# Optimization experiments

Measured on AMD Instinct MI355X. Metric: run time of the kernel, lower is better.

The kernel has to match this reference:

```python
import jax, jax.numpy as jnp
import numpy as np

N_NODES = 200000
N_EDGES = 6400000
IN_CH, HID, OUT_CH = 14, 16, 2


def gcn_conv(x, W, b, src, dst, n_nodes):
    """GCNConv with self-loops and symmetric normalization (PyG defaults).

    out[i] = sum_{j->i} d[i]^-1/2 d[j]^-1/2 (xW)[j] + d[i]^-1 (xW)[i] + b,
    where d = degree(A + I) computed on the target index.
    """
    h = x @ W  # [N, F_out]
    ones = jnp.ones((src.shape[0],), dtype=x.dtype)
    deg = jax.ops.segment_sum(ones, dst, num_segments=n_nodes) + 1.0  # +1 self-loop
    dinv = jax.lax.rsqrt(deg)  # [N]
    norm = dinv[src] * dinv[dst]  # [E]
    msg = h[src] * norm[:, None]  # [E, F_out] -- dominant memory traffic
    agg = jax.ops.segment_sum(msg, dst, num_segments=n_nodes)
    self_loop = h * (dinv * dinv)[:, None]
    return agg + self_loop + b


def setup_inputs() -> dict:
    key = jax.random.key(0)
    k1, k2, k3, k4, k5 = jax.random.split(key, 5)
    x = jax.random.normal(k1, (N_NODES, IN_CH), dtype=jnp.float32)
    edge_index = jax.random.randint(k2, (2, N_EDGES), 0, N_NODES, dtype=jnp.int64)
    edge_attr = jax.random.normal(k3, (N_EDGES, 1), dtype=jnp.float32)  # unused by GCNConv
    s = 1.0 / np.sqrt(IN_CH)
    W1 = jax.random.uniform(k4, (IN_CH, HID), jnp.float32, -s, s)
    b1 = jnp.zeros((HID,), jnp.float32)
    s2 = 1.0 / np.sqrt(HID)
    W2 = jax.random.uniform(k5, (HID, OUT_CH), jnp.float32, -s2, s2)
    b2 = jnp.zeros((OUT_CH,), jnp.float32)
    return {"x": x, "edge_index": edge_index, "edge_attr": edge_attr,
            "W1": W1, "b1": b1, "W2": W2, "b2": b2}


def reference(x, edge_index, edge_attr, W1, b1, W2, b2):
    src, dst = edge_index[0], edge_index[1]
    n = x.shape[0]
    h = jax.nn.relu(gcn_conv(x, W1, b1, src, dst, n))
    # F.dropout(training=self.training) is identity in eval mode
    out = gcn_conv(h, W2, b2, src, dst, n)
    return out
```

## Files before the change

kernel.cpp:

```cpp
#include <hip/hip_runtime.h>
#include <hip/hip_fp16.h>


constexpr int NN = 200000;
constexpr int NE = 6400000;
constexpr int IC = 14;
constexpr int HC = 16;
constexpr int OC = 2;

constexpr int NBK = 392;
constexpr int NSUB = 8;
constexpr int SCAP = 2816;
constexpr int NSEG = NSUB * NBK;
constexpr int CCAP = NSUB * SCAP;
constexpr int SPT = (SCAP + 1023) / 1024;
constexpr int TILE = 5120;
constexpr int BTH = 512;
constexpr int IPT = TILE / BTH;
constexpr int IPT2 = IPT / 2;
constexpr int NTILE = NE / TILE;
constexpr int OVFCAP = 65536;
constexpr int NB = (NN + 255) / 256;
constexpr int NAGG = NN / 64;
constexpr int GSTR = 16;

typedef unsigned long long ull;
typedef float f4v __attribute__((ext_vector_type(4)));

__device__ __forceinline__ int phase_of(unsigned src) {
    return src >= 100000u ? (src >= 150000u ? 3 : 2) : (src >= 50000u ? 1 : 0);
}

__global__ void k_init(int* __restrict__ gcur, const void* __restrict__ ei,
                       int* __restrict__ flag) {
    int i = blockIdx.x * blockDim.x + threadIdx.x;
    if (i < NSEG) gcur[i * GSTR] = i * SCAP;
    else if (i == NSEG) gcur[i * GSTR] = 0;
    if (i == 500) {
        const ull* p = (const ull*)ei;
        ull acc = 0ULL;
        for (int k = 0; k < 64; ++k) acc |= (p[k] >> 32);
        *flag = (acc == 0ULL) ? 1 : 0;
    }
}

__global__ __launch_bounds__(BTH, 8) void k_binA(const void* __restrict__ ei,
                                                 const int* __restrict__ flag,
                                                 int* __restrict__ gcur,
                                                 unsigned* __restrict__ binned,
                                                 ull* __restrict__ ovf) {
    __shared__ int hist[NBK];
    __shared__ int lofs[NBK];
    __shared__ int gofs[NBK];
    __shared__ int wsum[BTH / 64];
    __shared__ unsigned stage[TILE];

    int t = threadIdx.x;
    int fl = *flag;
    int tile0 = blockIdx.x * TILE;
    int segbase = (blockIdx.x & (NSUB - 1)) * NBK;

    if (t < NBK) hist[t] = 0;
    __syncthreads();

    unsigned pk[IPT];
    unsigned ra[IPT];
#pragma unroll
    for (int k = 0; k < IPT2; ++k) {
        int e = tile0 + k * (2 * BTH) + 2 * t;
        int d0, d1, s0, s1;
        if (fl) {
            ulonglong2 dd = *(const ulonglong2*)((const long long*)ei + NE + e);
            ulonglong2 ss = *(const ulonglong2*)((const long long*)ei + e);
            d0 = (int)dd.x;
            d1 = (int)dd.y;
            s0 = (int)ss.x;
            s1 = (int)ss.y;
        } else {
            uint2 dd = *(const uint2*)((const int*)ei + NE + e);
            uint2 ss = *(const uint2*)((const int*)ei + e);
            d0 = (int)dd.x;
            d1 = (int)dd.y;
            s0 = (int)ss.x;
            s1 = (int)ss.y;
        }
        int b0 = d0 >> 9, b1 = d1 >> 9;
        int r0 = atomicAdd(&hist[b0], 1);
        int r1 = atomicAdd(&hist[b1], 1);
        pk[2 * k] = ((unsigned)(d0 & 511) << 18) | (unsigned)s0;
        pk[2 * k + 1] = ((unsigned)(d1 & 511) << 18) | (unsigned)s1;
        ra[2 * k] = ((unsigned)r0 << 9) | (unsigned)b0;
        ra[2 * k + 1] = ((unsigned)r1 << 9) | (unsigned)b1;
    }
    __syncthreads();

    int h0 = 0, h1 = 0, p = 0;
    if (t < NBK / 2) {
        h0 = hist[2 * t];
        h1 = hist[2 * t + 1];
        p = h0 + h1;
    }
    int lane = t & 63;
    int w = t >> 6;
    int incl = p;
#pragma unroll
    for (int off = 1; off < 64; off <<= 1) {
        int v = __shfl_up(incl, off, 64);
        if (lane >= off) incl += v;
    }
    if (lane == 63) wsum[w] = incl;
    __syncthreads();
    int wbase = 0;
#pragma unroll
    for (int ww = 0; ww < BTH / 64; ++ww) wbase += (ww < w) ? wsum[ww] : 0;
    int ex = wbase + incl - p;
    if (t < NBK / 2) {
        lofs[2 * t] = ex;
        lofs[2 * t + 1] = ex + h0;
    }
    if (t < NBK) gofs[t] = atomicAdd(&gcur[(segbase + t) * GSTR], hist[t]);
    __syncthreads();

#pragma unroll
    for (int k = 0; k < IPT; ++k) {
        int b = (int)(ra[k] & 511u);
        int r = (int)(ra[k] >> 9);
        stage[lofs[b] + r] = pk[k];
    }
    __syncthreads();

    for (int i = t; i < TILE; i += BTH) {
        int b = (i * 313) >> 12;
        if (b > NBK - 1) b = NBK - 1;
        while (b < NBK - 1 && lofs[b + 1] <= i) ++b;
        while (lofs[b] > i) --b;
        unsigned pack = stage[i];
        int seg = segbase + b;
        int dest = gofs[b] + (i - lofs[b]);
        if (dest < (seg + 1) * SCAP) {
            binned[dest] = pack;
        } else {
            int op = atomicAdd(&gcur[NSEG * GSTR], 1);
            if (op < OVFCAP) {
                int d = (b << 9) | (int)(pack >> 18);
                int s = (int)(pack & 0x3FFFF);
                ovf[op] = ((ull)d << 32) | (unsigned)s;
            }
        }
    }
}

__global__ __launch_bounds__(1024, 4) void k_sort(const int* __restrict__ gcur,
                                                  const unsigned* __restrict__ binned,
                                                  const ull* __restrict__ ovf,
                                                  unsigned* __restrict__ csr,
                                                  float* __restrict__ dinv,
                                                  int* __restrict__ rsg,
                                                  unsigned* __restrict__ spl) {
    __shared__ int cnt[2048];
    __shared__ int excl[2048];
    __shared__ int wsum[16];
    __shared__ int nseg[NSUB];
    __shared__ unsigned stage[CCAP];
    int b = blockIdx.x;
    int t = threadIdx.x;
    cnt[t] = 0;
    cnt[t + 1024] = 0;
    if (t < NSUB) {
        int seg = t * NBK + b;
        nseg[t] = min(gcur[seg * GSTR] - seg * SCAP, SCAP);
    }
    __syncthreads();
    int nov = min(gcur[NSEG * GSTR], OVFCAP);

    unsigned srcv[NSUB * SPT];
    unsigned rkv[NSUB * SPT];
#pragma unroll
    for (int s = 0; s < NSUB; ++s) {
        int n = nseg[s];
        int sb = (s * NBK + b) * SCAP;
#pragma unroll
        for (int k = 0; k < SPT; ++k) {
            int i = k * 1024 + t;
            rkv[s * SPT + k] = 0xFFFFFFFFu;
            if (i < n) {
                unsigned pack = binned[sb + i];
                unsigned src = pack & 0x3FFFFu;
                int key = ((int)(pack >> 18) << 2) | phase_of(src);
                int r = atomicAdd(&cnt[key], 1);
                srcv[s * SPT + k] = src;
                rkv[s * SPT + k] = ((unsigned)r << 11) | (unsigned)key;
            }
        }
    }
    __syncthreads();

    int h0 = cnt[2 * t];
    int h1 = cnt[2 * t + 1];
    int p = h0 + h1;
    int lane = t & 63;
    int w = t >> 6;
    int incl = p;
#pragma unroll
    for (int off = 1; off < 64; off <<= 1) {
        int v = __shfl_up(incl, off, 64);
        if (lane >= off) incl += v;
    }
    if (lane == 63) wsum[w] = incl;
    __syncthreads();
    int wbase = 0;
#pragma unroll
    for (int ww = 0; ww < 16; ++ww) wbase += (ww < w) ? wsum[ww] : 0;
    int ex = wbase + incl - p;
    excl[2 * t] = ex;
    excl[2 * t + 1] = ex + h0;
    __syncthreads();

#pragma unroll
    for (int c = 0; c < NSUB * SPT; ++c) {
        unsigned rk = rkv[c];
        if (rk != 0xFFFFFFFFu) {
            int key = (int)(rk & 0x7FFu);
            int r = (int)(rk >> 11);
            stage[excl[key] + r] = srcv[c];
        }
    }

    if (t < 512) {
        int g = (b << 9) + t;
        if (g < NN) {
            int c0 = cnt[4 * t];
            int c1 = cnt[4 * t + 1];
            int c2 = cnt[4 * t + 2];
            int c3 = cnt[4 * t + 3];
            int extra = 0;
            for (int k = 0; k < nov; ++k) extra += ((int)(ovf[k] >> 32) == g);
            dinv[g] = rsqrtf((float)(c0 + c1 + c2 + c3 + extra) + 1.0f);
            rsg[g] = b * CCAP + excl[4 * t];
            spl[g] = (unsigned)c0 | ((unsigned)c1 << 8) |
                     ((unsigned)c2 << 16) | ((unsigned)c3 << 24);
        }
    }
    __syncthreads();

    int total = excl[2047] + cnt[2047];
    int tot4 = (total + 3) >> 2;
    const uint4* st4 = (const uint4*)stage;
    uint4* csr4 = (uint4*)(csr + (size_t)b * CCAP);
#pragma unroll
    for (int k = 0; k < (CCAP / 4 + 1023) / 1024; ++k) {
        int i4 = k * 1024 + t;
        if (i4 < tot4) csr4[i4] = st4[i4];
    }
}

__global__ void k_prep(const float* __restrict__ x, const float* __restrict__ dinv,
                       __half* __restrict__ xph) {
    int i = blockIdx.x * blockDim.x + threadIdx.x;
    if (i >= NN * 16) return;
    int node = i >> 4;
    int c = i & 15;
    float v = (c < IC) ? dinv[node] * x[node * IC + c] : 0.0f;
    xph[i] = __float2half(v);
}

__global__ __launch_bounds__(256) void k_agg1(const int* __restrict__ rsg,
                                              const unsigned* __restrict__ spl,
                                              const unsigned* __restrict__ csr,
                                              const __half* __restrict__ xph,
                                              float* __restrict__ partial,
                                              int pbase, int acc) {
    int t = threadIdx.x;
    int q2 = blockIdx.x & 1;
    int ph = pbase + q2;
    int blk = blockIdx.x >> 1;
    int g = t >> 2;
    int qq = t & 3;
    int i = blk * 64 + g;
    unsigned sp = spl[i];
    int c0 = (int)(sp & 255u);
    int c1 = (int)((sp >> 8) & 255u);
    int c2 = (int)((sp >> 16) & 255u);
    int c3 = (int)(sp >> 24);
    int off = (ph > 0 ? c0 : 0) + (ph > 1 ? c1 : 0) + (ph > 2 ? c2 : 0);
    int len = ph == 0 ? c0 : ph == 1 ? c1 : ph == 2 ? c2 : c3;
    int beg = rsg[i] + off;
    int end = beg + len;

    float ax = 0.0f, ay = 0.0f, az = 0.0f, aw = 0.0f;
    int j = beg;
    for (; j + 1 < end; j += 2) {
        int s0 = csr[j];
        int s1 = csr[j + 1];
        uint2 u0 = *(const uint2*)(xph + (size_t)s0 * 16 + 4 * qq);
        uint2 u1 = *(const uint2*)(xph + (size_t)s1 * 16 + 4 * qq);
        float2 f0 = __half22float2(*(__half2*)&u0.x);
        float2 f1 = __half22float2(*(__half2*)&u0.y);
        float2 f2 = __half22float2(*(__half2*)&u1.x);
        float2 f3 = __half22float2(*(__half2*)&u1.y);
        ax += f0.x + f2.x;
        ay += f0.y + f2.y;
        az += f1.x + f3.x;
        aw += f1.y + f3.y;
    }
    if (j < end) {
        int s0 = csr[j];
        uint2 u0 = *(const uint2*)(xph + (size_t)s0 * 16 + 4 * qq);
        float2 f0 = __half22float2(*(__half2*)&u0.x);
        float2 f1 = __half22float2(*(__half2*)&u0.y);
        ax += f0.x;
        ay += f0.y;
        az += f1.x;
        aw += f1.y;
    }
    f4v r = {ax, ay, az, aw};
    float* dst = partial + ((size_t)q2 * NN + i) * 16 + 4 * qq;
    if (acc) {
        f4v o = __builtin_nontemporal_load((const f4v*)dst);
        r += o;
    }
    __builtin_nontemporal_store(r, (f4v*)dst);
}

__global__ __launch_bounds__(256) void k_mlp(const float* __restrict__ partial,
                                             const __half* __restrict__ xph,
                                             const int* __restrict__ gcur,
                                             const ull* __restrict__ ovf,
                                             const float* __restrict__ dinv,
                                             const float* __restrict__ W1,
                                             const float* __restrict__ b1,
                                             const float* __restrict__ W2,
                                             const float* __restrict__ b2,
                                             float2* __restrict__ h2bp,
                                             float2* __restrict__ selfout) {
    __shared__ float sW1[IC * HC];
    __shared__ float sb1[HC];
    __shared__ float sW2[HC * OC];
    __shared__ float sb2[OC];
    int t = threadIdx.x;
    if (t < IC * HC) sW1[t] = W1[t];
    if (t < HC) sb1[t] = b1[t];
    if (t < HC * OC) sW2[t] = W2[t];
    if (t < OC) sb2[t] = b2[t];
    __syncthreads();

    int i = blockIdx.x * 256 + t;
    if (i >= NN) return;

    float dv = dinv[i];
    const float4* p0 = (const float4*)(partial + (size_t)i * 16);
    const float4* p1 = (const float4*)(partial + ((size_t)NN + i) * 16);
    const uint2* sp = (const uint2*)(xph + (size_t)i * 16);

    float agg[16];
#pragma unroll
    for (int c4 = 0; c4 < 4; ++c4) {
        float4 a = p0[c4];
        float4 b = p1[c4];
        uint2 u = sp[c4];
        float2 s0 = __half22float2(*(__half2*)&u.x);
        float2 s1 = __half22float2(*(__half2*)&u.y);
        agg[4 * c4 + 0] = a.x + b.x + s0.x;
        agg[4 * c4 + 1] = a.y + b.y + s0.y;
        agg[4 * c4 + 2] = a.z + b.z + s1.x;
        agg[4 * c4 + 3] = a.w + b.w + s1.y;
    }

    int nov = min(gcur[NSEG * GSTR], OVFCAP);
    for (int k = 0; k < nov; ++k) {
        ull e = ovf[k];
        if ((int)(e >> 32) == i) {
            int s = (int)(e & 0xFFFFFFFFu);
            for (int c = 0; c < IC; ++c)
                agg[c] += __half2float(xph[(size_t)s * 16 + c]);
        }
    }

    float tt[IC];
#pragma unroll
    for (int c = 0; c < IC; ++c) tt[c] = dv * agg[c];

    float r[HC];
#pragma unroll
    for (int f = 0; f < HC; ++f) {
        float a = sb1[f];
#pragma unroll
        for (int c = 0; c < IC; ++c) a = fmaf(tt[c], sW1[c * HC + f], a);
        r[f] = fmaxf(a, 0.0f);
    }

    float o0 = 0.0f, o1 = 0.0f;
#pragma unroll
    for (int f = 0; f < HC; ++f) {
        o0 = fmaf(r[f], sW2[f * OC + 0], o0);
        o1 = fmaf(r[f], sW2[f * OC + 1], o1);
    }
    h2bp[i] = make_float2(o0 * dv, o1 * dv);
    selfout[i] = make_float2(o0 * dv * dv + sb2[0], o1 * dv * dv + sb2[1]);
}

__global__ __launch_bounds__(256) void k_agg2(const int* __restrict__ rsg,
                                              const unsigned* __restrict__ spl,
                                              const unsigned* __restrict__ csr,
                                              const int* __restrict__ gcur,
                                              const ull* __restrict__ ovf,
                                              const float* __restrict__ dinv,
                                              const float2* __restrict__ h2bp,
                                              const float2* __restrict__ selfout,
                                              float2* __restrict__ out) {
    int tt = blockIdx.x * 256 + threadIdx.x;
    int i = tt >> 2;
    int h = tt & 3;
    if (i >= NN) return;
    unsigned sp = spl[i];
    int tot = (int)(sp & 255u) + (int)((sp >> 8) & 255u) +
              (int)((sp >> 16) & 255u) + (int)(sp >> 24);
    int beg = rsg[i];
    int end = beg + tot;
    float ax = 0.0f, ay = 0.0f;
    int j = beg + h;
    for (; j + 4 < end; j += 8) {
        int s0 = csr[j];
        int s1 = csr[j + 4];
        float2 h0 = h2bp[s0];
        float2 h1 = h2bp[s1];
        ax += h0.x + h1.x;
        ay += h0.y + h1.y;
    }
    if (j < end) {
        float2 h0 = h2bp[csr[j]];
        ax += h0.x;
        ay += h0.y;
    }
    ax += __shfl_xor(ax, 1);
    ay += __shfl_xor(ay, 1);
    ax += __shfl_xor(ax, 2);
    ay += __shfl_xor(ay, 2);
    if (h == 0) {
        int nov = min(gcur[NSEG * GSTR], OVFCAP);
        for (int k = 0; k < nov; ++k) {
            ull e = ovf[k];
            if ((int)(e >> 32) == i) {
                float2 hh = h2bp[(int)(e & 0xFFFFFFFFu)];
                ax += hh.x;
                ay += hh.y;
            }
        }
        float dv = dinv[i];
        float2 so = selfout[i];
        out[i] = make_float2(so.x + dv * ax, so.y + dv * ay);
    }
}

extern "C" void kernel_launch(void* const* d_in, const int* in_sizes, int n_in,
                              void* d_out, int out_size, void* d_ws, size_t ws_size,
                              hipStream_t stream) {
    const float* x = (const float*)d_in[0];
    const void* ei = d_in[1];
    const float* W1 = (const float*)d_in[3];
    const float* b1 = (const float*)d_in[4];
    const float* W2 = (const float*)d_in[5];
    const float* b2 = (const float*)d_in[6];
    float* out = (float*)d_out;

    ull* ovf = (ull*)d_ws;
    int* gcur = (int*)(ovf + OVFCAP);
    int* flag = gcur + (NSEG + 1) * GSTR;
    int* rsg = flag + 4;
    unsigned* spl = (unsigned*)(rsg + NN);
    float* dinv = (float*)(spl + NN);
    __half* xph = (__half*)(dinv + NN);
    float2* h2bp = (float2*)(xph + (size_t)NN * 16);
    float2* selfout = h2bp + NN;
    unsigned* binned = (unsigned*)(selfout + NN);
    float* partial = (float*)binned;
    unsigned* csr = binned + (size_t)NSEG * SCAP;

    k_init<<<(NSEG + 1 + 255) / 256, 256, 0, stream>>>(gcur, ei, flag);
    k_binA<<<NTILE, BTH, 0, stream>>>(ei, flag, gcur, binned, ovf);
    k_sort<<<NBK, 1024, 0, stream>>>(gcur, binned, ovf, csr, dinv, rsg, spl);
    k_prep<<<(NN * 16 + 255) / 256, 256, 0, stream>>>(x, dinv, xph);
    k_agg1<<<2 * NAGG, 256, 0, stream>>>(rsg, spl, csr, xph, partial, 0, 0);
    k_agg1<<<2 * NAGG, 256, 0, stream>>>(rsg, spl, csr, xph, partial, 2, 1);
    k_mlp<<<NB, 256, 0, stream>>>(partial, xph, gcur, ovf, dinv, W1, b1, W2, b2,
                                  h2bp, selfout);
    k_agg2<<<(NN * 4 + 255) / 256, 256, 0, stream>>>(rsg, spl, csr, gcur, ovf, dinv,
                                                     h2bp, selfout, (float2*)out);
}
```

Before: 308.5 us.

## Make binning and aggregation XCC-aware via hardware XCC id and atomic work claiming

The binning kernel now picks its sub-segment from the hardware XCC id instead of the block index, so each chiplet writes into its own bin region. The aggregation kernel replaces static block-to-phase mapping with an atomic work counter: blocks on XCCs 0-3 prefer one source-range phase and XCCs 4-7 the other, falling back to the other counter when theirs is exhausted. The goal is to keep each half of the gathered feature table resident in the local L2/cache of the chiplets processing it. This adds per-block atomics and a block-wide sync, and the number of blocks per bin region now depends on how the hardware distributes work across XCCs, so a skewed distribution could overflow a region's fixed capacity.

```diff
diff --git a/kernel.cpp b/kernel.cpp
--- a/kernel.cpp
+++ b/kernel.cpp
@@ -31,11 +31,17 @@
     return src >= 100000u ? (src >= 150000u ? 3 : 2) : (src >= 50000u ? 1 : 0);
 }
 
+__device__ __forceinline__ int xcc_id() {
+    int x;
+    asm volatile("s_getreg_b32 %0, hwreg(HW_REG_XCC_ID)" : "=s"(x));
+    return x & 7;
+}
+
 __global__ void k_init(int* __restrict__ gcur, const void* __restrict__ ei,
                        int* __restrict__ flag) {
     int i = blockIdx.x * blockDim.x + threadIdx.x;
     if (i < NSEG) gcur[i * GSTR] = i * SCAP;
-    else if (i == NSEG) gcur[i * GSTR] = 0;
+    else if (i <= NSEG + 4) gcur[i * GSTR] = 0;
     if (i == 500) {
         const ull* p = (const ull*)ei;
         ull acc = 0ULL;
@@ -58,7 +64,7 @@
     int t = threadIdx.x;
     int fl = *flag;
     int tile0 = blockIdx.x * TILE;
-    int segbase = (blockIdx.x & (NSUB - 1)) * NBK;
+    int segbase = xcc_id() * NBK;
 
     if (t < NBK) hist[t] = 0;
     __syncthreads();
@@ -269,11 +275,28 @@
                                               const unsigned* __restrict__ csr,
                                               const __half* __restrict__ xph,
                                               float* __restrict__ partial,
-                                              int pbase, int acc) {
+                                              int* __restrict__ gcur,
+                                              int pbase, int cbase, int acc) {
+    __shared__ int sw[2];
     int t = threadIdx.x;
-    int q2 = blockIdx.x & 1;
+    if (t == 0) {
+        int* cur = gcur + (NSEG + 1 + cbase) * GSTR;
+        int pref = (xcc_id() >> 2) & 1;
+        int idx = atomicAdd(&cur[pref * GSTR], 1);
+        int p = pref;
+        if (idx >= NAGG) {
+            p = pref ^ 1;
+            idx = atomicAdd(&cur[p * GSTR], 1);
+        }
+        sw[0] = idx;
+        sw[1] = p;
+    }
+    __syncthreads();
+    int blk = sw[0];
+    if (blk >= NAGG) return;
+    int q2 = sw[1];
     int ph = pbase + q2;
-    int blk = blockIdx.x >> 1;
+
     int g = t >> 2;
     int qq = t & 3;
     int i = blk * 64 + g;
@@ -314,7 +337,7 @@
         aw += f1.y;
     }
     f4v r = {ax, ay, az, aw};
-    float* dst = partial + ((size_t)q2 * NN + i) * 16 + 4 * qq;
+    float* dst = partial + ((size_t)(ph & 1) * NN + i) * 16 + 4 * qq;
     if (acc) {
         f4v o = __builtin_nontemporal_load((const f4v*)dst);
         r += o;
@@ -465,7 +488,7 @@
 
     ull* ovf = (ull*)d_ws;
     int* gcur = (int*)(ovf + OVFCAP);
-    int* flag = gcur + (NSEG + 1) * GSTR;
+    int* flag = gcur + (NSEG + 5) * GSTR;
     int* rsg = flag + 4;
     unsigned* spl = (unsigned*)(rsg + NN);
     float* dinv = (float*)(spl + NN);
@@ -476,12 +499,12 @@
     float* partial = (float*)binned;
     unsigned* csr = binned + (size_t)NSEG * SCAP;
 
-    k_init<<<(NSEG + 1 + 255) / 256, 256, 0, stream>>>(gcur, ei, flag);
+    k_init<<<(NSEG + 5 + 255) / 256, 256, 0, stream>>>(gcur, ei, flag);
     k_binA<<<NTILE, BTH, 0, stream>>>(ei, flag, gcur, binned, ovf);
     k_sort<<<NBK, 1024, 0, stream>>>(gcur, binned, ovf, csr, dinv, rsg, spl);
     k_prep<<<(NN * 16 + 255) / 256, 256, 0, stream>>>(x, dinv, xph);
-    k_agg1<<<2 * NAGG, 256, 0, stream>>>(rsg, spl, csr, xph, partial, 0, 0);
-    k_agg1<<<2 * NAGG, 256, 0, stream>>>(rsg, spl, csr, xph, partial, 2, 1);
+    k_agg1<<<2 * NAGG, 256, 0, stream>>>(rsg, spl, csr, xph, partial, gcur, 0, 0, 0);
+    k_agg1<<<2 * NAGG, 256, 0, stream>>>(rsg, spl, csr, xph, partial, gcur, 2, 2, 1);
     k_mlp<<<NB, 256, 0, stream>>>(partial, xph, gcur, ovf, dinv, W1, b1, W2, b2,
                                   h2bp, selfout);
     k_agg2<<<(NN * 4 + 255) / 256, 256, 0, stream>>>(rsg, spl, csr, gcur, ovf, dinv,
```

New measurement: 354.2 us. 14.8% more time.

## Fuse second aggregation pass with MLP and bin edges by XCC id

Applied to the files above, without the earlier changes.

The second layer-1 aggregation launch (source-range phases 2 and 3) is merged with the per-node MLP kernel into one kernel. Four threads per node gather the remaining phases, add the two stored partials and the self term, and compute the 16-wide hidden layer and 2-wide output cooperatively via shared memory and lane shuffles. This drops one launch and the read-modify-write of the partial buffer. Separately, the binning kernel now picks its sub-segment from the hardware XCC id instead of the block index, meant to keep atomic cursor traffic local to one chiplet. In exchange, the phase 2 and 3 gather no longer splits into two blocks per node group, so that part of the work runs with less parallelism.

```diff
diff --git a/kernel.cpp b/kernel.cpp
--- a/kernel.cpp
+++ b/kernel.cpp
@@ -20,7 +20,6 @@
 constexpr int IPT2 = IPT / 2;
 constexpr int NTILE = NE / TILE;
 constexpr int OVFCAP = 65536;
-constexpr int NB = (NN + 255) / 256;
 constexpr int NAGG = NN / 64;
 constexpr int GSTR = 16;
 
@@ -29,13 +28,19 @@
 
 __device__ __forceinline__ int phase_of(unsigned src) {
     return src >= 100000u ? (src >= 150000u ? 3 : 2) : (src >= 50000u ? 1 : 0);
+}
+
+__device__ __forceinline__ int xcc_id() {
+    int x;
+    asm volatile("s_getreg_b32 %0, hwreg(HW_REG_XCC_ID)" : "=s"(x));
+    return x & 7;
 }
 
 __global__ void k_init(int* __restrict__ gcur, const void* __restrict__ ei,
                        int* __restrict__ flag) {
     int i = blockIdx.x * blockDim.x + threadIdx.x;
     if (i < NSEG) gcur[i * GSTR] = i * SCAP;
-    else if (i == NSEG) gcur[i * GSTR] = 0;
+    else if (i <= NSEG + 4) gcur[i * GSTR] = 0;
     if (i == 500) {
         const ull* p = (const ull*)ei;
         ull acc = 0ULL;
@@ -58,7 +63,7 @@
     int t = threadIdx.x;
     int fl = *flag;
     int tile0 = blockIdx.x * TILE;
-    int segbase = (blockIdx.x & (NSUB - 1)) * NBK;
+    int segbase = xcc_id() * NBK;
 
     if (t < NBK) hist[t] = 0;
     __syncthreads();
@@ -268,11 +273,9 @@
                                               const unsigned* __restrict__ spl,
                                               const unsigned* __restrict__ csr,
                                               const __half* __restrict__ xph,
-                                              float* __restrict__ partial,
-                                              int pbase, int acc) {
+                                              float* __restrict__ partial) {
     int t = threadIdx.x;
     int q2 = blockIdx.x & 1;
-    int ph = pbase + q2;
     int blk = blockIdx.x >> 1;
     int g = t >> 2;
     int qq = t & 3;
@@ -280,12 +283,8 @@
     unsigned sp = spl[i];
     int c0 = (int)(sp & 255u);
     int c1 = (int)((sp >> 8) & 255u);
-    int c2 = (int)((sp >> 16) & 255u);
-    int c3 = (int)(sp >> 24);
-    int off = (ph > 0 ? c0 : 0) + (ph > 1 ? c1 : 0) + (ph > 2 ? c2 : 0);
-    int len = ph == 0 ? c0 : ph == 1 ? c1 : ph == 2 ? c2 : c3;
-    int beg = rsg[i] + off;
-    int end = beg + len;
+    int beg = rsg[i] + (q2 ? c0 : 0);
+    int end = beg + (q2 ? c1 : c0);
 
     float ax = 0.0f, ay = 0.0f, az = 0.0f, aw = 0.0f;
     int j = beg;
@@ -314,89 +313,122 @@
         aw += f1.y;
     }
     f4v r = {ax, ay, az, aw};
-    float* dst = partial + ((size_t)q2 * NN + i) * 16 + 4 * qq;
-    if (acc) {
-        f4v o = __builtin_nontemporal_load((const f4v*)dst);
-        r += o;
-    }
-    __builtin_nontemporal_store(r, (f4v*)dst);
-}
-
-__global__ __launch_bounds__(256) void k_mlp(const float* __restrict__ partial,
-                                             const __half* __restrict__ xph,
-                                             const int* __restrict__ gcur,
-                                             const ull* __restrict__ ovf,
-                                             const float* __restrict__ dinv,
-                                             const float* __restrict__ W1,
-                                             const float* __restrict__ b1,
-                                             const float* __restrict__ W2,
-                                             const float* __restrict__ b2,
-                                             float2* __restrict__ h2bp,
-                                             float2* __restrict__ selfout) {
+    __builtin_nontemporal_store(r, (f4v*)(partial + ((size_t)q2 * NN + i) * 16 + 4 * qq));
+}
+
+__global__ __launch_bounds__(256) void k_agg1m(const int* __restrict__ rsg,
+                                               const unsigned* __restrict__ spl,
+                                               const unsigned* __restrict__ csr,
+                                               const __half* __restrict__ xph,
+                                               const float* __restrict__ partial,
+                                               const int* __restrict__ gcur,
+                                               const ull* __restrict__ ovf,
+                                               const float* __restrict__ dinv,
+                                               const float* __restrict__ W1,
+                                               const float* __restrict__ b1,
+                                               const float* __restrict__ W2,
+                                               const float* __restrict__ b2,
+                                               float2* __restrict__ h2bp,
+                                               float2* __restrict__ selfout) {
     __shared__ float sW1[IC * HC];
     __shared__ float sb1[HC];
     __shared__ float sW2[HC * OC];
     __shared__ float sb2[OC];
+    __shared__ float sAgg[64][17];
     int t = threadIdx.x;
     if (t < IC * HC) sW1[t] = W1[t];
     if (t < HC) sb1[t] = b1[t];
     if (t < HC * OC) sW2[t] = W2[t];
     if (t < OC) sb2[t] = b2[t];
-    __syncthreads();
-
-    int i = blockIdx.x * 256 + t;
-    if (i >= NN) return;
-
-    float dv = dinv[i];
-    const float4* p0 = (const float4*)(partial + (size_t)i * 16);
-    const float4* p1 = (const float4*)(partial + ((size_t)NN + i) * 16);
-    const uint2* sp = (const uint2*)(xph + (size_t)i * 16);
-
-    float agg[16];
-#pragma unroll
-    for (int c4 = 0; c4 < 4; ++c4) {
-        float4 a = p0[c4];
-        float4 b = p1[c4];
-        uint2 u = sp[c4];
-        float2 s0 = __half22float2(*(__half2*)&u.x);
-        float2 s1 = __half22float2(*(__half2*)&u.y);
-        agg[4 * c4 + 0] = a.x + b.x + s0.x;
-        agg[4 * c4 + 1] = a.y + b.y + s0.y;
-        agg[4 * c4 + 2] = a.z + b.z + s1.x;
-        agg[4 * c4 + 3] = a.w + b.w + s1.y;
-    }
+
+    int g = t >> 2;
+    int qq = t & 3;
+    int i = blockIdx.x * 64 + g;
+    unsigned sp = spl[i];
+    int c0 = (int)(sp & 255u);
+    int c1 = (int)((sp >> 8) & 255u);
+    int c2 = (int)((sp >> 16) & 255u);
+    int c3 = (int)(sp >> 24);
+    int beg = rsg[i] + c0 + c1;
+    int end = beg + c2 + c3;
+
+    float ax = 0.0f, ay = 0.0f, az = 0.0f, aw = 0.0f;
+    int j = beg;
+    for (; j + 1 < end; j += 2) {
+        int s0 = csr[j];
+        int s1 = csr[j + 1];
+        uint2 u0 = *(const uint2*)(xph + (size_t)s0 * 16 + 4 * qq);
+        uint2 u1 = *(const uint2*)(xph + (size_t)s1 * 16 + 4 * qq);
+        float2 f0 = __half22float2(*(__half2*)&u0.x);
+        float2 f1 = __half22float2(*(__half2*)&u0.y);
+        float2 f2 = __half22float2(*(__half2*)&u1.x);
+        float2 f3 = __half22float2(*(__half2*)&u1.y);
+        ax += f0.x + f2.x;
+        ay += f0.y + f2.y;
+        az += f1.x + f3.x;
+        aw += f1.y + f3.y;
+    }
+    if (j < end) {
+        int s0 = csr[j];
+        uint2 u0 = *(const uint2*)(xph + (size_t)s0 * 16 + 4 * qq);
+        float2 f0 = __half22float2(*(__half2*)&u0.x);
+        float2 f1 = __half22float2(*(__half2*)&u0.y);
+        ax += f0.x;
+        ay += f0.y;
+        az += f1.x;
+        aw += f1.y;
+    }
+
+    f4v a0 = __builtin_nontemporal_load((const f4v*)(partial + (size_t)i * 16 + 4 * qq));
+    f4v a1 = __builtin_nontemporal_load(
+        (const f4v*)(partial + ((size_t)NN + i) * 16 + 4 * qq));
+    uint2 us = *(const uint2*)(xph + (size_t)i * 16 + 4 * qq);
+    float2 sx = __half22float2(*(__half2*)&us.x);
+    float2 sy = __half22float2(*(__half2*)&us.y);
+    float v0 = ax + a0.x + a1.x + sx.x;
+    float v1 = ay + a0.y + a1.y + sx.y;
+    float v2 = az + a0.z + a1.z + sy.x;
+    float v3 = aw + a0.w + a1.w + sy.y;
 
     int nov = min(gcur[NSEG * GSTR], OVFCAP);
     for (int k = 0; k < nov; ++k) {
         ull e = ovf[k];
         if ((int)(e >> 32) == i) {
             int s = (int)(e & 0xFFFFFFFFu);
-            for (int c = 0; c < IC; ++c)
-                agg[c] += __half2float(xph[(size_t)s * 16 + c]);
-        }
-    }
-
-    float tt[IC];
-#pragma unroll
-    for (int c = 0; c < IC; ++c) tt[c] = dv * agg[c];
-
-    float r[HC];
-#pragma unroll
-    for (int f = 0; f < HC; ++f) {
+            int ch = 4 * qq;
+            v0 += __half2float(xph[(size_t)s * 16 + ch]);
+            v1 += __half2float(xph[(size_t)s * 16 + ch + 1]);
+            v2 += __half2float(xph[(size_t)s * 16 + ch + 2]);
+            v3 += __half2float(xph[(size_t)s * 16 + ch + 3]);
+        }
+    }
+
+    float dv = dinv[i];
+    sAgg[g][4 * qq + 0] = dv * v0;
+    sAgg[g][4 * qq + 1] = dv * v1;
+    sAgg[g][4 * qq + 2] = dv * v2;
+    sAgg[g][4 * qq + 3] = dv * v3;
+    __syncthreads();
+
+    float o0 = 0.0f, o1 = 0.0f;
+#pragma unroll
+    for (int f4 = 0; f4 < 4; ++f4) {
+        int f = 4 * qq + f4;
         float a = sb1[f];
 #pragma unroll
-        for (int c = 0; c < IC; ++c) a = fmaf(tt[c], sW1[c * HC + f], a);
-        r[f] = fmaxf(a, 0.0f);
-    }
-
-    float o0 = 0.0f, o1 = 0.0f;
-#pragma unroll
-    for (int f = 0; f < HC; ++f) {
-        o0 = fmaf(r[f], sW2[f * OC + 0], o0);
-        o1 = fmaf(r[f], sW2[f * OC + 1], o1);
-    }
-    h2bp[i] = make_float2(o0 * dv, o1 * dv);
-    selfout[i] = make_float2(o0 * dv * dv + sb2[0], o1 * dv * dv + sb2[1]);
+        for (int c = 0; c < IC; ++c) a = fmaf(sAgg[g][c], sW1[c * HC + f], a);
+        a = fmaxf(a, 0.0f);
+        o0 = fmaf(a, sW2[f * OC + 0], o0);
+        o1 = fmaf(a, sW2[f * OC + 1], o1);
+    }
+    o0 += __shfl_xor(o0, 1);
+    o1 += __shfl_xor(o1, 1);
+    o0 += __shfl_xor(o0, 2);
+    o1 += __shfl_xor(o1, 2);
+    if (qq == 0) {
+        h2bp[i] = make_float2(o0 * dv, o1 * dv);
+        selfout[i] = make_float2(o0 * dv * dv + sb2[0], o1 * dv * dv + sb2[1]);
+    }
 }
 
 __global__ __launch_bounds__(256) void k_agg2(const int* __restrict__ rsg,
@@ -465,7 +497,7 @@
 
     ull* ovf = (ull*)d_ws;
     int* gcur = (int*)(ovf + OVFCAP);
-    int* flag = gcur + (NSEG + 1) * GSTR;
+    int* flag = gcur + (NSEG + 5) * GSTR;
     int* rsg = flag + 4;
     unsigned* spl = (unsigned*)(rsg + NN);
     float* dinv = (float*)(spl + NN);
@@ -476,14 +508,13 @@
     float* partial = (float*)binned;
     unsigned* csr = binned + (size_t)NSEG * SCAP;
 
-    k_init<<<(NSEG + 1 + 255) / 256, 256, 0, stream>>>(gcur, ei, flag);
+    k_init<<<(NSEG + 5 + 255) / 256, 256, 0, stream>>>(gcur, ei, flag);
     k_binA<<<NTILE, BTH, 0, stream>>>(ei, flag, gcur, binned, ovf);
     k_sort<<<NBK, 1024, 0, stream>>>(gcur, binned, ovf, csr, dinv, rsg, spl);
     k_prep<<<(NN * 16 + 255) / 256, 256, 0, stream>>>(x, dinv, xph);
-    k_agg1<<<2 * NAGG, 256, 0, stream>>>(rsg, spl, csr, xph, partial, 0, 0);
-    k_agg1<<<2 * NAGG, 256, 0, stream>>>(rsg, spl, csr, xph, partial, 2, 1);
-    k_mlp<<<NB, 256, 0, stream>>>(partial, xph, gcur, ovf, dinv, W1, b1, W2, b2,
-                                  h2bp, selfout);
+    k_agg1<<<2 * NAGG, 256, 0, stream>>>(rsg, spl, csr, xph, partial);
+    k_agg1m<<<NAGG, 256, 0, stream>>>(rsg, spl, csr, xph, partial, gcur, ovf, dinv,
+                                      W1, b1, W2, b2, h2bp, selfout);
     k_agg2<<<(NN * 4 + 255) / 256, 256, 0, stream>>>(rsg, spl, csr, gcur, ovf, dinv,
                                                      h2bp, selfout, (float2*)out);
 }
```

After: 299.0 us. 1.03x faster.
